# Kernel optimization log

Hardware: AMD Instinct MI355X
Metric: run time of the kernel (lower is better)

The kernel has to match this reference:

```python
import jax, jax.numpy as jnp
import numpy as np

T, H, E, I = 512, 2048, 8, 1024


def setup_inputs() -> dict:
    key = jax.random.key(0)
    k1, k2, k3, k4 = jax.random.split(key, 4)
    x = jax.random.normal(k1, (T, H), dtype=jnp.float32)
    router_logits = jax.random.normal(k2, (T, E), dtype=jnp.float32)
    # w13 stacks [gate; up] along the output dim: [E, 2I, H]
    w13_weight = jax.random.normal(k3, (E, 2 * I, H), dtype=jnp.float32) * (1.0 / np.sqrt(H))
    w2_weight = jax.random.normal(k4, (E, H, I), dtype=jnp.float32) * (1.0 / np.sqrt(I))
    return {"x": x, "router_logits": router_logits, "w13_weight": w13_weight,
            "w2_weight": w2_weight, "top_k": 2}


def reference(x, router_logits, w13_weight, w2_weight, top_k):
    t, h = x.shape
    e = router_logits.shape[-1]
    # select_experts: softmax -> top_k -> renormalize
    probs = jax.nn.softmax(router_logits.astype(jnp.float32), axis=-1)  # [T, E]
    topk_w, topk_ids = jax.lax.top_k(probs, top_k)                      # [T, K]
    topk_w = topk_w / jnp.sum(topk_w, axis=-1, keepdims=True)
    # dense combine weights [T, E]; zero for unselected experts
    combine = jnp.zeros((t, e), dtype=x.dtype).at[
        jnp.arange(t)[:, None], topk_ids
    ].add(topk_w.astype(x.dtype))
    # grouped expert SwiGLU MLP (computed densely over experts, masked by combine)
    gu = jnp.einsum('th,enh->ten', x, w13_weight)   # [T, E, 2I]
    i = gu.shape[-1] // 2
    gate, up = gu[..., :i], gu[..., i:]
    act = jax.nn.silu(gate) * up                    # [T, E, I]
    y = jnp.einsum('tei,ehi->teh', act, w2_weight)  # [T, E, H]
    return jnp.einsum('teh,te->th', y, combine)     # weighted combine [T, H]
```

## Files before the change

kernel.cpp:

```cpp
#include <hip/hip_runtime.h>
#include <hip/hip_bf16.h>

#define T_TOK 512
#define H_DIM 2048
#define E_NUM 8
#define I_DIM 1024

typedef __attribute__((ext_vector_type(8))) short short8;
typedef __attribute__((ext_vector_type(4))) float f32x4;

__device__ __forceinline__ unsigned short f2bf(float f) {
    unsigned int u = __float_as_uint(f);
    u += 0x7fff + ((u >> 16) & 1);
    return (unsigned short)(u >> 16);
}

__device__ __forceinline__ short8 cvt8(float4 a, float4 b) {
    union { short8 s; __hip_bfloat162 h[4]; } u;
    u.h[0] = __float22bfloat162_rn(make_float2(a.x, a.y));
    u.h[1] = __float22bfloat162_rn(make_float2(a.z, a.w));
    u.h[2] = __float22bfloat162_rn(make_float2(b.x, b.y));
    u.h[3] = __float22bfloat162_rn(make_float2(b.z, b.w));
    return u.s;
}

__device__ __forceinline__ void gload_lds16(const void* g, void* l) {
    __builtin_amdgcn_global_load_lds(
        (const __attribute__((address_space(1))) void*)g,
        (__attribute__((address_space(3))) void*)l, 16, 0, 0);
}

__global__ __launch_bounds__(512) void routing_kernel(
    const float* __restrict__ logits,
    int* __restrict__ count, int* __restrict__ bucket,
    float* __restrict__ pair_w)
{
    int t = threadIdx.x;
    if (t < E_NUM) count[t] = 0;
    __syncthreads();

    float p[E_NUM];
    float m = -INFINITY;
#pragma unroll
    for (int e = 0; e < E_NUM; ++e) {
        p[e] = logits[t * E_NUM + e];
        m = fmaxf(m, p[e]);
    }
#pragma unroll
    for (int e = 0; e < E_NUM; ++e) p[e] = expf(p[e] - m);
    int i0 = 0;
#pragma unroll
    for (int e = 1; e < E_NUM; ++e) if (p[e] > p[i0]) i0 = e;
    int i1 = (i0 == 0) ? 1 : 0;
#pragma unroll
    for (int e = 0; e < E_NUM; ++e) if (e != i0 && p[e] > p[i1]) i1 = e;
    float denom = p[i0] + p[i1];
    pair_w[2 * t + 0] = p[i0] / denom;
    pair_w[2 * t + 1] = p[i1] / denom;

    int pos0 = atomicAdd(&count[i0], 1);
    bucket[i0 * T_TOK + pos0] = 2 * t + 0;
    int pos1 = atomicAdd(&count[i1], 1);
    bucket[i1 * T_TOK + pos1] = 2 * t + 1;
}

__global__ __launch_bounds__(256) void gemm1_silu_kernel(
    const float* __restrict__ x, const float* __restrict__ w13,
    const int* __restrict__ count, const int* __restrict__ bucket,
    __hip_bfloat16* __restrict__ act)
{
    const int e   = blockIdx.z;
    const int n_e = count[e];
    const int m0  = blockIdx.y * 64;
    if (m0 >= n_e) return;
    const int n0  = blockIdx.x * 64;

    __shared__ float lds[2][3 * 64 * 32];

    const int tid  = threadIdx.x;
    const int lane = tid & 63;
    const int wid  = tid >> 6;
    const int fr   = lane & 15;
    const int fq   = lane >> 4;
    const int wr   = wid >> 1;
    const int wc   = wid & 1;

    const int srow = lane >> 3;
    const int slot = lane & 7;

    const float *aptr[2], *gptr[2], *uptr[2];
#pragma unroll
    for (int ii = 0; ii < 2; ++ii) {
        int r   = 16 * wid + 8 * ii + srow;
        int gsl = slot ^ (r & 7);
        int tok = bucket[e * T_TOK + min(m0 + r, n_e - 1)] >> 1;
        aptr[ii] = x + (size_t)tok * H_DIM + gsl * 4;
        gptr[ii] = w13 + ((size_t)e * (2 * I_DIM) + n0 + r) * H_DIM + gsl * 4;
        uptr[ii] = w13 + ((size_t)e * (2 * I_DIM) + I_DIM + n0 + r) * H_DIM + gsl * 4;
    }

    auto stage = [&](int kb, int buf) {
        float* b = lds[buf];
#pragma unroll
        for (int ii = 0; ii < 2; ++ii) {
            int rb = (16 * wid + 8 * ii) * 32;
            gload_lds16(aptr[ii] + kb, b + rb);
            gload_lds16(gptr[ii] + kb, b + 2048 + rb);
            gload_lds16(uptr[ii] + kb, b + 4096 + rb);
        }
    };

    f32x4 accg[2][2] = {};
    f32x4 accu[2][2] = {};
    short8 a[2], bg[2], bu[2];

    auto readfrags = [&](const float* b) {
#pragma unroll
        for (int m = 0; m < 2; ++m) {
            int r  = wr * 32 + m * 16 + fr;
            int s0 = (fq * 2) ^ (r & 7);
            float4 q0 = *(const float4*)(b + r * 32 + s0 * 4);
            float4 q1 = *(const float4*)(b + r * 32 + (s0 ^ 1) * 4);
            a[m] = cvt8(q0, q1);
        }
#pragma unroll
        for (int n = 0; n < 2; ++n) {
            int r  = wc * 32 + n * 16 + fr;
            int s0 = (fq * 2) ^ (r & 7);
            float4 g0 = *(const float4*)(b + 2048 + r * 32 + s0 * 4);
            float4 g1 = *(const float4*)(b + 2048 + r * 32 + (s0 ^ 1) * 4);
            bg[n] = cvt8(g0, g1);
            float4 u0 = *(const float4*)(b + 4096 + r * 32 + s0 * 4);
            float4 u1 = *(const float4*)(b + 4096 + r * 32 + (s0 ^ 1) * 4);
            bu[n] = cvt8(u0, u1);
        }
    };

    auto domfma = [&]() {
#pragma unroll
        for (int m = 0; m < 2; ++m)
#pragma unroll
            for (int n = 0; n < 2; ++n) {
                accg[m][n] = __builtin_amdgcn_mfma_f32_16x16x32_bf16(a[m], bg[n], accg[m][n], 0, 0, 0);
                accu[m][n] = __builtin_amdgcn_mfma_f32_16x16x32_bf16(a[m], bu[n], accu[m][n], 0, 0, 0);
            }
    };

    stage(0, 0);
#pragma unroll 2
    for (int t = 0; t < 63; ++t) {
        stage((t + 1) * 32, (t + 1) & 1);
        asm volatile("s_waitcnt vmcnt(6)" ::: "memory");
        __builtin_amdgcn_s_barrier();
        readfrags(lds[t & 1]);
        asm volatile("s_waitcnt lgkmcnt(0)" ::: "memory");
        __builtin_amdgcn_s_barrier();
        domfma();
    }
    asm volatile("s_waitcnt vmcnt(0)" ::: "memory");
    __builtin_amdgcn_s_barrier();
    readfrags(lds[1]);
    domfma();

#pragma unroll
    for (int m = 0; m < 2; ++m) {
#pragma unroll
        for (int j = 0; j < 4; ++j) {
            int r = m0 + wr * 32 + m * 16 + fq * 4 + j;
            if (r < n_e) {
                int pid = bucket[e * T_TOK + r];
                __hip_bfloat16* arow = act + (size_t)pid * I_DIM;
#pragma unroll
                for (int n = 0; n < 2; ++n) {
                    float g = accg[m][n][j];
                    float u = accu[m][n][j];
                    float sg = g / (1.f + expf(-g));
                    unsigned short v = f2bf(sg * u);
                    int col = n0 + wc * 32 + n * 16 + fr;
                    *(unsigned short*)(arow + col) = v;
                }
            }
        }
    }
}

__global__ __launch_bounds__(256) void gemm2_kernel(
    const __hip_bfloat16* __restrict__ act, const float* __restrict__ w2,
    const int* __restrict__ count, const int* __restrict__ bucket,
    float* __restrict__ y)
{
    const int e   = blockIdx.z;
    const int n_e = count[e];
    const int m0  = blockIdx.y * 64;
    if (m0 >= n_e) return;
    const int h0  = blockIdx.x * 64;

    __shared__ unsigned short sA[2][64 * 64];
    __shared__ float sB[2][64 * 64];

    const int tid  = threadIdx.x;
    const int lane = tid & 63;
    const int wid  = tid >> 6;
    const int fr   = lane & 15;
    const int fq   = lane >> 4;
    const int wr   = wid >> 1;
    const int wc   = wid & 1;

    const __hip_bfloat16* a2ptr[2];
#pragma unroll
    for (int ii = 0; ii < 2; ++ii) {
        int r   = 16 * wid + 8 * ii + (lane >> 3);
        int gsl = (lane & 7) ^ (r & 7);
        int pid = bucket[e * T_TOK + min(m0 + r, n_e - 1)];
        a2ptr[ii] = act + (size_t)pid * I_DIM + gsl * 8;
    }
    const float* b2ptr[4];
#pragma unroll
    for (int i = 0; i < 4; ++i) {
        int r   = 16 * wid + 4 * i + (lane >> 4);
        int gsl = (lane & 15) ^ (r & 7);
        b2ptr[i] = w2 + ((size_t)e * H_DIM + h0 + r) * I_DIM + gsl * 4;
    }

    auto stage = [&](int kb, int buf) {
#pragma unroll
        for (int ii = 0; ii < 2; ++ii)
            gload_lds16(a2ptr[ii] + kb, &sA[buf][(16 * wid + 8 * ii) * 64]);
#pragma unroll
        for (int i = 0; i < 4; ++i)
            gload_lds16(b2ptr[i] + kb, &sB[buf][(16 * wid + 4 * i) * 64]);
    };

    f32x4 acc[2][2] = {};
    short8 a[2][2], bf[2][2];

    auto readfrags = [&](int buf) {
#pragma unroll
        for (int kk = 0; kk < 2; ++kk) {
#pragma unroll
            for (int m = 0; m < 2; ++m) {
                int r = wr * 32 + m * 16 + fr;
                int g = (kk * 4 + fq) ^ (r & 7);
                a[kk][m] = *(const short8*)&sA[buf][r * 64 + g * 8];
            }
#pragma unroll
            for (int n = 0; n < 2; ++n) {
                int r  = wc * 32 + n * 16 + fr;
                int s0 = (kk * 8 + fq * 2) ^ (r & 7);
                float4 g0 = *(const float4*)&sB[buf][r * 64 + s0 * 4];
                float4 g1 = *(const float4*)&sB[buf][r * 64 + (s0 ^ 1) * 4];
                bf[kk][n] = cvt8(g0, g1);
            }
        }
    };

    auto domfma = [&]() {
#pragma unroll
        for (int kk = 0; kk < 2; ++kk)
#pragma unroll
            for (int m = 0; m < 2; ++m)
#pragma unroll
                for (int n = 0; n < 2; ++n)
                    acc[m][n] = __builtin_amdgcn_mfma_f32_16x16x32_bf16(a[kk][m], bf[kk][n], acc[m][n], 0, 0, 0);
    };

    stage(0, 0);
#pragma unroll 2
    for (int t = 0; t < 15; ++t) {
        stage((t + 1) * 64, (t + 1) & 1);
        asm volatile("s_waitcnt vmcnt(6)" ::: "memory");
        __builtin_amdgcn_s_barrier();
        readfrags(t & 1);
        asm volatile("s_waitcnt lgkmcnt(0)" ::: "memory");
        __builtin_amdgcn_s_barrier();
        domfma();
    }
    asm volatile("s_waitcnt vmcnt(0)" ::: "memory");
    __builtin_amdgcn_s_barrier();
    readfrags(1);
    domfma();

#pragma unroll
    for (int m = 0; m < 2; ++m) {
#pragma unroll
        for (int j = 0; j < 4; ++j) {
            int r = m0 + wr * 32 + m * 16 + fq * 4 + j;
            if (r < n_e) {
                int pid = bucket[e * T_TOK + r];
                float* yrow = y + (size_t)pid * H_DIM;
#pragma unroll
                for (int n = 0; n < 2; ++n)
                    yrow[h0 + wc * 32 + n * 16 + fr] = acc[m][n][j];
            }
        }
    }
}

__global__ __launch_bounds__(256) void combine_kernel(
    const float* __restrict__ y, const float* __restrict__ pair_w,
    float* __restrict__ out)
{
    int idx = blockIdx.x * 256 + threadIdx.x;
    int t = idx >> 9;
    int c = idx & 511;
    float w0 = pair_w[2 * t + 0];
    float w1 = pair_w[2 * t + 1];
    float4 y0 = ((const float4*)(y + (size_t)(2 * t + 0) * H_DIM))[c];
    float4 y1 = ((const float4*)(y + (size_t)(2 * t + 1) * H_DIM))[c];
    float4 o;
    o.x = w0 * y0.x + w1 * y1.x;
    o.y = w0 * y0.y + w1 * y1.y;
    o.z = w0 * y0.z + w1 * y1.z;
    o.w = w0 * y0.w + w1 * y1.w;
    ((float4*)(out + (size_t)t * H_DIM))[c] = o;
}

extern "C" void kernel_launch(void* const* d_in, const int* in_sizes, int n_in,
                              void* d_out, int out_size, void* d_ws, size_t ws_size,
                              hipStream_t stream) {
    const float* x      = (const float*)d_in[0];
    const float* logits = (const float*)d_in[1];
    const float* w13    = (const float*)d_in[2];
    const float* w2     = (const float*)d_in[3];
    float* out = (float*)d_out;

    int*   count  = (int*)d_ws;
    int*   bucket = count + E_NUM;
    float* pair_w = (float*)(bucket + E_NUM * T_TOK);
    __hip_bfloat16* act = (__hip_bfloat16*)(pair_w + 2 * T_TOK);
    float* ybuf   = (float*)(act + (size_t)2 * T_TOK * I_DIM);

    routing_kernel<<<1, 512, 0, stream>>>(logits, count, bucket, pair_w);
    gemm1_silu_kernel<<<dim3(I_DIM / 64, T_TOK / 64, E_NUM), 256, 0, stream>>>(
        x, w13, count, bucket, act);
    gemm2_kernel<<<dim3(H_DIM / 64, T_TOK / 64, E_NUM), 256, 0, stream>>>(
        act, w2, count, bucket, ybuf);
    combine_kernel<<<(T_TOK * (H_DIM / 4)) / 256, 256, 0, stream>>>(
        ybuf, pair_w, out);
}
```

Before: 95.78 us.

## Pre-convert x to bf16, halve N tiles, deepen pipeline to four stages

Adds a kernel that converts x to bf16 once, so gemm1 loads half the activation bytes and no longer converts A fragments in its inner loop. Both expert GEMMs shrink their N tile from 64 to 32, which doubles the grid to give more blocks for occupancy and parallelism. Both switch from double-buffered to four-deep LDS buffering with matching vmcnt waits. In exchange there is an extra launch and more reloading of the A tile across N blocks, and each block does less MFMA work per barrier.

```diff
diff --git a/kernel.cpp b/kernel.cpp
--- a/kernel.cpp
+++ b/kernel.cpp
@@ -30,6 +30,15 @@
         (__attribute__((address_space(3))) void*)l, 16, 0, 0);
 }
 
+__global__ __launch_bounds__(256) void xcvt_kernel(
+    const float* __restrict__ x, unsigned short* __restrict__ xb)
+{
+    int i = (blockIdx.x * 256 + threadIdx.x) * 8;
+    float4 v0 = *(const float4*)(x + i);
+    float4 v1 = *(const float4*)(x + i + 4);
+    *(short8*)(xb + i) = cvt8(v0, v1);
+}
+
 __global__ __launch_bounds__(512) void routing_kernel(
     const float* __restrict__ logits,
     int* __restrict__ count, int* __restrict__ bucket,
@@ -65,7 +74,7 @@
 }
 
 __global__ __launch_bounds__(256) void gemm1_silu_kernel(
-    const float* __restrict__ x, const float* __restrict__ w13,
+    const unsigned short* __restrict__ xb, const float* __restrict__ w13,
     const int* __restrict__ count, const int* __restrict__ bucket,
     __hip_bfloat16* __restrict__ act)
 {
@@ -73,9 +82,11 @@
     const int n_e = count[e];
     const int m0  = blockIdx.y * 64;
     if (m0 >= n_e) return;
-    const int n0  = blockIdx.x * 64;
-
-    __shared__ float lds[2][3 * 64 * 32];
+    const int n0  = blockIdx.x * 32;
+
+    __shared__ unsigned short sA[4][64 * 32];
+    __shared__ float sG[4][32 * 32];
+    __shared__ float sU[4][32 * 32];
 
     const int tid  = threadIdx.x;
     const int lane = tid & 63;
@@ -85,82 +96,52 @@
     const int wr   = wid >> 1;
     const int wc   = wid & 1;
 
-    const int srow = lane >> 3;
-    const int slot = lane & 7;
-
-    const float *aptr[2], *gptr[2], *uptr[2];
-#pragma unroll
-    for (int ii = 0; ii < 2; ++ii) {
-        int r   = 16 * wid + 8 * ii + srow;
-        int gsl = slot ^ (r & 7);
-        int tok = bucket[e * T_TOK + min(m0 + r, n_e - 1)] >> 1;
-        aptr[ii] = x + (size_t)tok * H_DIM + gsl * 4;
-        gptr[ii] = w13 + ((size_t)e * (2 * I_DIM) + n0 + r) * H_DIM + gsl * 4;
-        uptr[ii] = w13 + ((size_t)e * (2 * I_DIM) + I_DIM + n0 + r) * H_DIM + gsl * 4;
-    }
+    const int arow = 16 * wid + (lane >> 2);
+    const int tok  = bucket[e * T_TOK + min(m0 + arow, n_e - 1)] >> 1;
+    const unsigned short* aptr = xb + (size_t)tok * H_DIM + (lane & 3) * 8;
+    const int grow = 8 * wid + (lane >> 3);
+    const int gs   = (lane & 7) ^ (lane >> 3);
+    const float* gptr = w13 + ((size_t)e * (2 * I_DIM) + n0 + grow) * H_DIM + gs * 4;
+    const float* uptr = w13 + ((size_t)e * (2 * I_DIM) + I_DIM + n0 + grow) * H_DIM + gs * 4;
 
     auto stage = [&](int kb, int buf) {
-        float* b = lds[buf];
-#pragma unroll
-        for (int ii = 0; ii < 2; ++ii) {
-            int rb = (16 * wid + 8 * ii) * 32;
-            gload_lds16(aptr[ii] + kb, b + rb);
-            gload_lds16(gptr[ii] + kb, b + 2048 + rb);
-            gload_lds16(uptr[ii] + kb, b + 4096 + rb);
+        gload_lds16(aptr + kb, &sA[buf][16 * wid * 32]);
+        gload_lds16(gptr + kb, &sG[buf][8 * wid * 32]);
+        gload_lds16(uptr + kb, &sU[buf][8 * wid * 32]);
+    };
+
+    f32x4 accg[2] = {};
+    f32x4 accu[2] = {};
+
+    stage(0, 0); stage(32, 1); stage(64, 2);
+
+    for (int t = 0; t < 64; ++t) {
+        stage(min((t + 3) * 32, 2016), (t + 3) & 3);
+        asm volatile("s_waitcnt vmcnt(9)" ::: "memory");
+        __builtin_amdgcn_s_barrier();
+
+        const int buf = t & 3;
+        short8 a[2], bg, bu;
+#pragma unroll
+        for (int m = 0; m < 2; ++m)
+            a[m] = *(const short8*)&sA[buf][(wr * 32 + m * 16 + fr) * 32 + fq * 8];
+        {
+            int r  = wc * 16 + fr;
+            int s0 = (fq * 2) ^ (r & 7);
+            const float* gb = &sG[buf][r * 32];
+            bg = cvt8(*(const float4*)(gb + s0 * 4), *(const float4*)(gb + (s0 ^ 1) * 4));
+            const float* ub = &sU[buf][r * 32];
+            bu = cvt8(*(const float4*)(ub + s0 * 4), *(const float4*)(ub + (s0 ^ 1) * 4));
         }
-    };
-
-    f32x4 accg[2][2] = {};
-    f32x4 accu[2][2] = {};
-    short8 a[2], bg[2], bu[2];
-
-    auto readfrags = [&](const float* b) {
-#pragma unroll
-        for (int m = 0; m < 2; ++m) {
-            int r  = wr * 32 + m * 16 + fr;
-            int s0 = (fq * 2) ^ (r & 7);
-            float4 q0 = *(const float4*)(b + r * 32 + s0 * 4);
-            float4 q1 = *(const float4*)(b + r * 32 + (s0 ^ 1) * 4);
-            a[m] = cvt8(q0, q1);
-        }
-#pragma unroll
-        for (int n = 0; n < 2; ++n) {
-            int r  = wc * 32 + n * 16 + fr;
-            int s0 = (fq * 2) ^ (r & 7);
-            float4 g0 = *(const float4*)(b + 2048 + r * 32 + s0 * 4);
-            float4 g1 = *(const float4*)(b + 2048 + r * 32 + (s0 ^ 1) * 4);
-            bg[n] = cvt8(g0, g1);
-            float4 u0 = *(const float4*)(b + 4096 + r * 32 + s0 * 4);
-            float4 u1 = *(const float4*)(b + 4096 + r * 32 + (s0 ^ 1) * 4);
-            bu[n] = cvt8(u0, u1);
-        }
-    };
-
-    auto domfma = [&]() {
-#pragma unroll
-        for (int m = 0; m < 2; ++m)
-#pragma unroll
-            for (int n = 0; n < 2; ++n) {
-                accg[m][n] = __builtin_amdgcn_mfma_f32_16x16x32_bf16(a[m], bg[n], accg[m][n], 0, 0, 0);
-                accu[m][n] = __builtin_amdgcn_mfma_f32_16x16x32_bf16(a[m], bu[n], accu[m][n], 0, 0, 0);
-            }
-    };
-
-    stage(0, 0);
-#pragma unroll 2
-    for (int t = 0; t < 63; ++t) {
-        stage((t + 1) * 32, (t + 1) & 1);
-        asm volatile("s_waitcnt vmcnt(6)" ::: "memory");
-        __builtin_amdgcn_s_barrier();
-        readfrags(lds[t & 1]);
         asm volatile("s_waitcnt lgkmcnt(0)" ::: "memory");
         __builtin_amdgcn_s_barrier();
-        domfma();
+
+        accg[0] = __builtin_amdgcn_mfma_f32_16x16x32_bf16(a[0], bg, accg[0], 0, 0, 0);
+        accg[1] = __builtin_amdgcn_mfma_f32_16x16x32_bf16(a[1], bg, accg[1], 0, 0, 0);
+        accu[0] = __builtin_amdgcn_mfma_f32_16x16x32_bf16(a[0], bu, accu[0], 0, 0, 0);
+        accu[1] = __builtin_amdgcn_mfma_f32_16x16x32_bf16(a[1], bu, accu[1], 0, 0, 0);
     }
     asm volatile("s_waitcnt vmcnt(0)" ::: "memory");
-    __builtin_amdgcn_s_barrier();
-    readfrags(lds[1]);
-    domfma();
 
 #pragma unroll
     for (int m = 0; m < 2; ++m) {
@@ -169,16 +150,11 @@
             int r = m0 + wr * 32 + m * 16 + fq * 4 + j;
             if (r < n_e) {
                 int pid = bucket[e * T_TOK + r];
-                __hip_bfloat16* arow = act + (size_t)pid * I_DIM;
-#pragma unroll
-                for (int n = 0; n < 2; ++n) {
-                    float g = accg[m][n][j];
-                    float u = accu[m][n][j];
-                    float sg = g / (1.f + expf(-g));
-                    unsigned short v = f2bf(sg * u);
-                    int col = n0 + wc * 32 + n * 16 + fr;
-                    *(unsigned short*)(arow + col) = v;
-                }
+                float g = accg[m][j];
+                float u = accu[m][j];
+                float sg = g / (1.f + expf(-g));
+                int col = n0 + wc * 16 + fr;
+                *(unsigned short*)(act + (size_t)pid * I_DIM + col) = f2bf(sg * u);
             }
         }
     }
@@ -193,10 +169,10 @@
     const int n_e = count[e];
     const int m0  = blockIdx.y * 64;
     if (m0 >= n_e) return;
-    const int h0  = blockIdx.x * 64;
-
-    __shared__ unsigned short sA[2][64 * 64];
-    __shared__ float sB[2][64 * 64];
+    const int h0  = blockIdx.x * 32;
+
+    __shared__ unsigned short sA[4][64 * 64];
+    __shared__ float sB[4][32 * 64];
 
     const int tid  = threadIdx.x;
     const int lane = tid & 63;
@@ -206,79 +182,67 @@
     const int wr   = wid >> 1;
     const int wc   = wid & 1;
 
-    const __hip_bfloat16* a2ptr[2];
-#pragma unroll
-    for (int ii = 0; ii < 2; ++ii) {
-        int r   = 16 * wid + 8 * ii + (lane >> 3);
+    const unsigned short* aptr[2];
+#pragma unroll
+    for (int i = 0; i < 2; ++i) {
+        int r   = 16 * wid + 8 * i + (lane >> 3);
         int gsl = (lane & 7) ^ (r & 7);
         int pid = bucket[e * T_TOK + min(m0 + r, n_e - 1)];
-        a2ptr[ii] = act + (size_t)pid * I_DIM + gsl * 8;
-    }
-    const float* b2ptr[4];
-#pragma unroll
-    for (int i = 0; i < 4; ++i) {
-        int r   = 16 * wid + 4 * i + (lane >> 4);
+        aptr[i] = (const unsigned short*)act + (size_t)pid * I_DIM + gsl * 8;
+    }
+    const float* bptr[2];
+#pragma unroll
+    for (int i = 0; i < 2; ++i) {
+        int r   = 8 * wid + 4 * i + (lane >> 4);
         int gsl = (lane & 15) ^ (r & 7);
-        b2ptr[i] = w2 + ((size_t)e * H_DIM + h0 + r) * I_DIM + gsl * 4;
+        bptr[i] = w2 + ((size_t)e * H_DIM + h0 + r) * I_DIM + gsl * 4;
     }
 
     auto stage = [&](int kb, int buf) {
 #pragma unroll
-        for (int ii = 0; ii < 2; ++ii)
-            gload_lds16(a2ptr[ii] + kb, &sA[buf][(16 * wid + 8 * ii) * 64]);
-#pragma unroll
-        for (int i = 0; i < 4; ++i)
-            gload_lds16(b2ptr[i] + kb, &sB[buf][(16 * wid + 4 * i) * 64]);
+        for (int i = 0; i < 2; ++i)
+            gload_lds16(aptr[i] + kb, &sA[buf][(16 * wid + 8 * i) * 64]);
+#pragma unroll
+        for (int i = 0; i < 2; ++i)
+            gload_lds16(bptr[i] + kb, &sB[buf][(8 * wid + 4 * i) * 64]);
     };
 
-    f32x4 acc[2][2] = {};
-    short8 a[2][2], bf[2][2];
-
-    auto readfrags = [&](int buf) {
+    f32x4 acc[2] = {};
+
+    stage(0, 0); stage(64, 1); stage(128, 2);
+
+    for (int t = 0; t < 16; ++t) {
+        stage(min((t + 3) * 64, 960), (t + 3) & 3);
+        asm volatile("s_waitcnt vmcnt(12)" ::: "memory");
+        __builtin_amdgcn_s_barrier();
+
+        const int buf = t & 3;
+        short8 a[2][2], b[2];
 #pragma unroll
         for (int kk = 0; kk < 2; ++kk) {
 #pragma unroll
             for (int m = 0; m < 2; ++m) {
-                int r = wr * 32 + m * 16 + fr;
-                int g = (kk * 4 + fq) ^ (r & 7);
-                a[kk][m] = *(const short8*)&sA[buf][r * 64 + g * 8];
+                int r    = wr * 32 + m * 16 + fr;
+                int slot = (kk * 4 + fq) ^ (r & 7);
+                a[kk][m] = *(const short8*)&sA[buf][r * 64 + slot * 8];
             }
-#pragma unroll
-            for (int n = 0; n < 2; ++n) {
-                int r  = wc * 32 + n * 16 + fr;
+            {
+                int r  = wc * 16 + fr;
                 int s0 = (kk * 8 + fq * 2) ^ (r & 7);
-                float4 g0 = *(const float4*)&sB[buf][r * 64 + s0 * 4];
-                float4 g1 = *(const float4*)&sB[buf][r * 64 + (s0 ^ 1) * 4];
-                bf[kk][n] = cvt8(g0, g1);
+                const float* bb = &sB[buf][r * 64];
+                b[kk] = cvt8(*(const float4*)(bb + s0 * 4), *(const float4*)(bb + (s0 ^ 1) * 4));
             }
         }
-    };
-
-    auto domfma = [&]() {
-#pragma unroll
-        for (int kk = 0; kk < 2; ++kk)
-#pragma unroll
-            for (int m = 0; m < 2; ++m)
-#pragma unroll
-                for (int n = 0; n < 2; ++n)
-                    acc[m][n] = __builtin_amdgcn_mfma_f32_16x16x32_bf16(a[kk][m], bf[kk][n], acc[m][n], 0, 0, 0);
-    };
-
-    stage(0, 0);
-#pragma unroll 2
-    for (int t = 0; t < 15; ++t) {
-        stage((t + 1) * 64, (t + 1) & 1);
-        asm volatile("s_waitcnt vmcnt(6)" ::: "memory");
-        __builtin_amdgcn_s_barrier();
-        readfrags(t & 1);
         asm volatile("s_waitcnt lgkmcnt(0)" ::: "memory");
         __builtin_amdgcn_s_barrier();
-        domfma();
+
+#pragma unroll
+        for (int kk = 0; kk < 2; ++kk)
+#pragma unroll
+            for (int m = 0; m < 2; ++m)
+                acc[m] = __builtin_amdgcn_mfma_f32_16x16x32_bf16(a[kk][m], b[kk], acc[m], 0, 0, 0);
     }
     asm volatile("s_waitcnt vmcnt(0)" ::: "memory");
-    __builtin_amdgcn_s_barrier();
-    readfrags(1);
-    domfma();
 
 #pragma unroll
     for (int m = 0; m < 2; ++m) {
@@ -287,10 +251,7 @@
             int r = m0 + wr * 32 + m * 16 + fq * 4 + j;
             if (r < n_e) {
                 int pid = bucket[e * T_TOK + r];
-                float* yrow = y + (size_t)pid * H_DIM;
-#pragma unroll
-                for (int n = 0; n < 2; ++n)
-                    yrow[h0 + wc * 32 + n * 16 + fr] = acc[m][n][j];
+                y[(size_t)pid * H_DIM + h0 + wc * 16 + fr] = acc[m][j];
             }
         }
     }
@@ -327,13 +288,15 @@
     int*   count  = (int*)d_ws;
     int*   bucket = count + E_NUM;
     float* pair_w = (float*)(bucket + E_NUM * T_TOK);
-    __hip_bfloat16* act = (__hip_bfloat16*)(pair_w + 2 * T_TOK);
-    float* ybuf   = (float*)(act + (size_t)2 * T_TOK * I_DIM);
-
+    unsigned short* xb = (unsigned short*)(pair_w + 2 * T_TOK);
+    __hip_bfloat16* act = (__hip_bfloat16*)(xb + (size_t)T_TOK * H_DIM);
+    float* ybuf   = (float*)((unsigned short*)act + (size_t)2 * T_TOK * I_DIM);
+
+    xcvt_kernel<<<(T_TOK * H_DIM / 8) / 256, 256, 0, stream>>>(x, xb);
     routing_kernel<<<1, 512, 0, stream>>>(logits, count, bucket, pair_w);
-    gemm1_silu_kernel<<<dim3(I_DIM / 64, T_TOK / 64, E_NUM), 256, 0, stream>>>(
-        x, w13, count, bucket, act);
-    gemm2_kernel<<<dim3(H_DIM / 64, T_TOK / 64, E_NUM), 256, 0, stream>>>(
+    gemm1_silu_kernel<<<dim3(I_DIM / 32, T_TOK / 64, E_NUM), 256, 0, stream>>>(
+        xb, w13, count, bucket, act);
+    gemm2_kernel<<<dim3(H_DIM / 32, T_TOK / 64, E_NUM), 256, 0, stream>>>(
         act, w2, count, bucket, ybuf);
     combine_kernel<<<(T_TOK * (H_DIM / 4)) / 256, 256, 0, stream>>>(
         ybuf, pair_w, out);
```

Result: slower. 101.8 us (+6.3%).
